# Performance work log

Hardware: AMD Instinct MI355X
Metric: run time of the kernel (lower is better)

## Reference

```python
import jax, jax.numpy as jnp
import numpy as np

NS = 0.4      # neighborhood_size
GS = 8        # grid_size
RNN = 128     # rnn_size
EMB = 64      # embedding_size
NMIX = 20     # nmixtures
N = 1024      # num pedestrians


def setup_inputs() -> dict:
    key = jax.random.key(0)
    ks = jax.random.split(key, 14)
    s = 0.05
    return {
        "xoff": jax.random.normal(ks[0], (N, 2)) * s,
        "xabs": jax.random.uniform(ks[1], (N, 2)),
        "h0": jax.random.normal(ks[2], (1, N, RNN)) * 0.1,
        "c0": jax.random.normal(ks[3], (1, N, RNN)) * 0.1,
        "W_emb": jax.random.normal(ks[4], (EMB, 2)) * s,
        "b_emb": jax.random.normal(ks[5], (EMB,)) * s,
        "W_soc": jax.random.normal(ks[6], (EMB, GS * GS * RNN)) * s,
        "b_soc": jax.random.normal(ks[7], (EMB,)) * s,
        "W_ih": jax.random.normal(ks[8], (4 * RNN, 2 * EMB)) * s,
        "W_hh": jax.random.normal(ks[9], (4 * RNN, RNN)) * s,
        "b_ih": jax.random.normal(ks[10], (4 * RNN,)) * s,
        "b_hh": jax.random.normal(ks[11], (4 * RNN,)) * s,
        "W_out": jax.random.normal(ks[12], (6 * NMIX, RNN)) * s,
        "b_out": jax.random.normal(ks[13], (6 * NMIX,)) * s,
    }


def grid_mask(xabs, dtype):
    # Vectorized getGridMask: [N, N, GS*GS] one-hot neighbor binning.
    x, y = xabs[:, 0], xabs[:, 1]
    dx = x[None, :] - (x[:, None] - NS / 2)  # other_x - width_low, [N, N]
    dy = y[None, :] - (y[:, None] - NS / 2)
    cx = jnp.floor(dx / NS * GS).astype(jnp.int32)
    cy = jnp.floor(dy / NS * GS).astype(jnp.int32)
    n = x.shape[0]
    valid = ((dx >= 0) & (dx < NS) & (dy >= 0) & (dy < NS)
             & (cx >= 0) & (cx < GS) & (cy >= 0) & (cy < GS)
             & ~jnp.eye(n, dtype=bool))
    cell = jnp.clip(cx + cy * GS, 0, GS * GS - 1)
    return jax.nn.one_hot(cell, GS * GS, dtype=dtype) * valid[..., None].astype(dtype)


def reference(xoff, xabs, h0, c0, W_emb, b_emb, W_soc, b_soc,
              W_ih, W_hh, b_ih, b_hh, W_out, b_out):
    n = xabs.shape[0]
    # predict_distance=True -> embed offsets
    emb = jax.nn.relu(xoff @ W_emb.T + b_emb)                 # [N, 64]
    grid = grid_mask(xabs, emb.dtype)                          # [N, N, 64]
    h = h0[0]                                                  # [N, 128]
    # getSocialTensor: scatter neighbor hidden states into grid bins
    social = jnp.einsum('nmg,mh->ngh', grid, h).reshape(n, GS * GS * RNN)
    pool = jax.nn.relu(social @ W_soc.T + b_soc)               # [N, 64]
    xin = jnp.concatenate([emb, pool], axis=-1)                # [N, 128]
    # single-step LSTM, torch gate order i, f, g, o
    gates = xin @ W_ih.T + h @ W_hh.T + b_ih + b_hh            # [N, 512]
    i, f, g, o = jnp.split(gates, 4, axis=-1)
    c = jax.nn.sigmoid(f) * c0[0] + jax.nn.sigmoid(i) * jnp.tanh(g)
    hn = jax.nn.sigmoid(o) * jnp.tanh(c)
    out = hn @ W_out.T + b_out                                 # [N, 120]
    mu1, mu2, ls1, ls2, rho, pi_logits = jnp.split(out, 6, axis=1)
    return (mu1, mu2, ls1, ls2, rho, pi_logits)
```

## Files before the change

### kernel.cpp

```cpp
#include <hip/hip_runtime.h>
#include <hip/hip_bf16.h>

#define NN_ 1024

#define U_WIHT   0
#define U_WHHT   65536
#define U_WOUT   131072
#define OFF_POOL 73728
#define U_HHI    278528
#define U_HLO    409600
#define U_SHI    540672
#define U_SLO    1064960
#define U_P      1589248

typedef __attribute__((ext_vector_type(8))) short short8;
typedef __attribute__((ext_vector_type(4))) float floatx4;

__device__ __forceinline__ float b2f_(unsigned short u) {
    return __uint_as_float(((unsigned)u) << 16);
}
__device__ __forceinline__ unsigned short f2bu(float f) {
    __hip_bfloat16 b = __float2bfloat16(f);
    return *(unsigned short*)&b;
}
__device__ __forceinline__ float ldin(const void* p, int i, int isbf) {
    return isbf ? b2f_(((const unsigned short*)p)[i]) : ((const float*)p)[i];
}
__device__ __forceinline__ int detect_bf16(const void* Wih, int tid) {
    unsigned wv = ((const unsigned*)Wih)[tid];
    unsigned e8 = (wv >> 7) & 0xFFu;
    return (__syncthreads_count((e8 >= 96u && e8 <= 134u) ? 1 : 0) > 128) ? 1 : 0;
}

__global__ void prep_kernel(const void* __restrict__ h0,
                            const void* __restrict__ Wsoc,
                            const void* __restrict__ Wih_det,
                            float* __restrict__ ws) {
    const int tid = threadIdx.x;
    const int isbf = detect_bf16(Wih_det, tid);
    unsigned short* u16 = (unsigned short*)ws;
    int t = blockIdx.x * 256 + tid;
    float x; int dhi, dlo;
    if (t < 131072) {
        x = ldin(h0, t, isbf);
        dhi = U_HHI + t; dlo = U_HLO + t;
    } else {
        int t2 = t - 131072;
        x = ldin(Wsoc, t2, isbf);
        dhi = U_SHI + t2; dlo = U_SLO + t2;
    }
    unsigned short hi = f2bu(x);
    u16[dhi] = hi;
    u16[dlo] = f2bu(x - b2f_(hi));
}

__global__ __launch_bounds__(256) void pgemm_kernel(float* __restrict__ ws,
                                                    int m0, int mcnt) {
    const unsigned short* u16 = (const unsigned short*)ws;
    const short* Hhi = (const short*)(u16 + U_HHI);
    const short* Hlo = (const short*)(u16 + U_HLO);
    const short* Shi = (const short*)(u16 + U_SHI);
    const short* Slo = (const short*)(u16 + U_SLO);
    unsigned short* P16 = (unsigned short*)ws + U_P;

    const int tid  = threadIdx.x;
    const int lane = tid & 63;
    const int wv   = tid >> 6;
    const int B    = blockIdx.y * 64 + blockIdx.x;
    const int mtiles = mcnt >> 4;
    const int mtile  = B % mtiles;
    const int cg     = B / mtiles;
    const int m = lane & 15;
    const int q = lane >> 4;
    const int abase = (m0 + mtile * 16 + m) * 128 + q * 8;
    short8 ah[4], al[4];
#pragma unroll
    for (int j = 0; j < 4; j++) {
        ah[j] = *(const short8*)(Hhi + abase + 32 * j);
        al[j] = *(const short8*)(Hlo + abase + 32 * j);
    }
    const int rowl = mtile * 16 + q * 4;
#pragma unroll
    for (int t = 0; t < 4; t++) {
        int n0 = cg * 256 + wv * 64 + t * 16;
        int nc = n0 + m;
        int e  = nc & 63, g = nc >> 6;
        int wb = e * 8192 + g * 128 + q * 8;
        short8 bh[4], bl[4];
#pragma unroll
        for (int j = 0; j < 4; j++) {
            bh[j] = *(const short8*)(Shi + wb + 32 * j);
            bl[j] = *(const short8*)(Slo + wb + 32 * j);
        }
        floatx4 c = {0.0f, 0.0f, 0.0f, 0.0f};
#pragma unroll
        for (int j = 0; j < 4; j++) c = __builtin_amdgcn_mfma_f32_16x16x32_bf16(ah[j], bh[j], c, 0, 0, 0);
#pragma unroll
        for (int j = 0; j < 4; j++) c = __builtin_amdgcn_mfma_f32_16x16x32_bf16(ah[j], bl[j], c, 0, 0, 0);
#pragma unroll
        for (int j = 0; j < 4; j++) c = __builtin_amdgcn_mfma_f32_16x16x32_bf16(al[j], bh[j], c, 0, 0, 0);
#pragma unroll
        for (int r = 0; r < 4; r++)
            P16[(rowl + r) * 4096 + n0 + m] = f2bu(c[r]);
    }
}

__global__ __launch_bounds__(256) void pool_kernel(const void* __restrict__ xabs,
                                                   const void* __restrict__ Wih,
                                                   const void* __restrict__ Whh,
                                                   const void* __restrict__ Wout,
                                                   float* __restrict__ ws,
                                                   int m0, int mcount, int first) {
    __shared__ int off[NN_];
    __shared__ int cnt_s;
    __shared__ float4 red4[16][16];
    const int tid = threadIdx.x;
    const int isbf = detect_bf16(Wih, tid);
    const int n = blockIdx.x;

    if (first && blockIdx.x < 144) {
        unsigned short* u16 = (unsigned short*)ws;
        int base = blockIdx.x * 1024;
        for (int i = tid; i < 1024; i += 256) {
            int t = base + i;
            float v;
            if (t < 65536)       { int k = t >> 9, j = t & 511;       v = ldin(Wih, j * 128 + k, isbf); }
            else if (t < 131072) { int t2 = t - 65536; int k = t2 >> 9, j = t2 & 511; v = ldin(Whh, j * 128 + k, isbf); }
            else                 { int t2 = t - 131072; int r = t2 >> 7, j = t2 & 127;
                                   v = (j < 120) ? ldin(Wout, j * 128 + r, isbf) : 0.0f; }
            u16[t] = f2bu(v);
        }
    }
    if (tid == 0) cnt_s = 0;
    __syncthreads();

    float xs = ldin(xabs, 2 * n, isbf)     - 0.2f;
    float ys = ldin(xabs, 2 * n + 1, isbf) - 0.2f;
    for (int i = tid; i < mcount; i += 256) {
        int m = m0 + i;
        float dx = ldin(xabs, 2 * m, isbf)     - xs;
        float dy = ldin(xabs, 2 * m + 1, isbf) - ys;
        int cx = (int)floorf(dx / 0.4f * 8.0f);
        int cy = (int)floorf(dy / 0.4f * 8.0f);
        bool valid = (dx >= 0.0f) && (dx < 0.4f) && (dy >= 0.0f) && (dy < 0.4f)
                  && (cx >= 0) && (cx < 8) && (cy >= 0) && (cy < 8) && (m != n);
        if (valid) {
            int idx = atomicAdd(&cnt_s, 1);
            off[idx] = i * 4096 + ((cy * 8 + cx) << 6);
        }
    }
    __syncthreads();
    const unsigned short* P16 = (const unsigned short*)ws + U_P;
    const int e4 = tid & 15, strm = tid >> 4;
    const int cc = cnt_s;
    float ax = 0.0f, ay = 0.0f, az = 0.0f, aw = 0.0f;
    for (int j = strm; j < cc; j += 16) {
        int o = off[j];
        ushort4 u = *(const ushort4*)(P16 + o + 4 * e4);
        ax += b2f_(u.x); ay += b2f_(u.y); az += b2f_(u.z); aw += b2f_(u.w);
    }
    red4[strm][e4] = make_float4(ax, ay, az, aw);
    __syncthreads();
    if (tid < 16) {
        float4 s = make_float4(0.0f, 0.0f, 0.0f, 0.0f);
#pragma unroll
        for (int s16 = 0; s16 < 16; s16++) {
            float4 r = red4[s16][tid];
            s.x += r.x; s.y += r.y; s.z += r.z; s.w += r.w;
        }
        float* pp = ws + OFF_POOL + n * 64 + 4 * tid;
        if (!first) { s.x += pp[0]; s.y += pp[1]; s.z += pp[2]; s.w += pp[3]; }
        *(float4*)pp = s;
    }
}

__global__ __launch_bounds__(256) void lstm_out_kernel(
        const void* __restrict__ xoff, const void* __restrict__ h0,
        const void* __restrict__ c0,   const void* __restrict__ W_emb,
        const void* __restrict__ b_emb, const void* __restrict__ b_soc,
        const void* __restrict__ b_ih, const void* __restrict__ b_hh,
        const void* __restrict__ b_out, const void* __restrict__ Wih_det,
        const float* __restrict__ ws, float* __restrict__ out) {
    __shared__ __align__(16) float xin[2][128];
    __shared__ __align__(16) float hs[2][128];
    __shared__ __align__(16) float gl[2][512];
    __shared__ __align__(16) float hnl[2][128];
    const int tid = threadIdx.x;
    const int isbf = detect_bf16(Wih_det, tid);
    const int n0 = blockIdx.x * 2;
    const unsigned short* u16 = (const unsigned short*)ws;
    if (tid < 128) {
        int nn = tid >> 6, e = tid & 63, n = n0 + nn;
        float v = fmaf(ldin(xoff, 2 * n, isbf),     ldin(W_emb, 2 * e, isbf),
                  fmaf(ldin(xoff, 2 * n + 1, isbf), ldin(W_emb, 2 * e + 1, isbf),
                       ldin(b_emb, e, isbf)));
        xin[nn][e] = fmaxf(v, 0.0f);
        xin[nn][64 + e] = fmaxf(ws[OFF_POOL + n * 64 + e] + ldin(b_soc, e, isbf), 0.0f);
    } else {
        int t = tid - 128;
    }
    {
        int nn = tid >> 7, k = tid & 127;
        hs[nn][k] = ldin(h0, (n0 + nn) * 128 + k, isbf);
    }
    __syncthreads();
    {
        const int j0 = 2 * tid, j1 = 2 * tid + 1;
        float ax[2] = {0, 0}, ay[2] = {0, 0};
        for (int k = 0; k < 128; k += 4) {
            union { float4 v; float f[4]; } xu[2], hu[2];
#pragma unroll
            for (int nn = 0; nn < 2; nn++) {
                xu[nn].v = *(const float4*)&xin[nn][k];
                hu[nn].v = *(const float4*)&hs[nn][k];
            }
#pragma unroll
            for (int kk = 0; kk < 4; kk++) {
                ushort2 wi = *(const ushort2*)(u16 + U_WIHT + (k + kk) * 512 + j0);
                ushort2 wh = *(const ushort2*)(u16 + U_WHHT + (k + kk) * 512 + j0);
                float wix = b2f_(wi.x), wiy = b2f_(wi.y);
                float whx = b2f_(wh.x), why = b2f_(wh.y);
#pragma unroll
                for (int nn = 0; nn < 2; nn++) {
                    float xk = xu[nn].f[kk], hk = hu[nn].f[kk];
                    ax[nn] = fmaf(xk, wix, ax[nn]); ax[nn] = fmaf(hk, whx, ax[nn]);
                    ay[nn] = fmaf(xk, wiy, ay[nn]); ay[nn] = fmaf(hk, why, ay[nn]);
                }
            }
        }
        float bb0 = ldin(b_ih, j0, isbf) + ldin(b_hh, j0, isbf);
        float bb1 = ldin(b_ih, j1, isbf) + ldin(b_hh, j1, isbf);
#pragma unroll
        for (int nn = 0; nn < 2; nn++) {
            gl[nn][j0] = ax[nn] + bb0;
            gl[nn][j1] = ay[nn] + bb1;
        }
    }
    __syncthreads();
    {
        int nn = tid >> 7, r = tid & 127;
        int n = n0 + nn;
        float iv = gl[nn][r], fv = gl[nn][r + 128], gv = gl[nn][r + 256], ov = gl[nn][r + 384];
        float si = 1.0f / (1.0f + expf(-iv));
        float sf = 1.0f / (1.0f + expf(-fv));
        float so = 1.0f / (1.0f + expf(-ov));
        float cc = sf * ldin(c0, n * 128 + r, isbf) + si * tanhf(gv);
        hnl[nn][r] = so * tanhf(cc);
    }
    __syncthreads();
    {
        int nn = tid >> 7, j = tid & 127;
        if (j < 120) {
            float acc = ldin(b_out, j, isbf);
            for (int r = 0; r < 128; r += 4) {
                float4 hq = *(const float4*)&hnl[nn][r];
                acc = fmaf(hq.x, b2f_(u16[U_WOUT + (r + 0) * 128 + j]), acc);
                acc = fmaf(hq.y, b2f_(u16[U_WOUT + (r + 1) * 128 + j]), acc);
                acc = fmaf(hq.z, b2f_(u16[U_WOUT + (r + 2) * 128 + j]), acc);
                acc = fmaf(hq.w, b2f_(u16[U_WOUT + (r + 3) * 128 + j]), acc);
            }
            int ch = j / 20, wc = j - ch * 20;
            out[ch * 20480 + (n0 + nn) * 20 + wc] = acc;
        }
    }
}

extern "C" void kernel_launch(void* const* d_in, const int* in_sizes, int n_in,
                              void* d_out, int out_size, void* d_ws, size_t ws_size,
                              hipStream_t stream) {
    const void* xoff  = d_in[0];
    const void* xabs  = d_in[1];
    const void* h0    = d_in[2];
    const void* c0    = d_in[3];
    const void* W_emb = d_in[4];
    const void* b_emb = d_in[5];
    const void* W_soc = d_in[6];
    const void* b_soc = d_in[7];
    const void* W_ih  = d_in[8];
    const void* W_hh  = d_in[9];
    const void* b_ih  = d_in[10];
    const void* b_hh  = d_in[11];
    const void* W_out = d_in[12];
    const void* b_out = d_in[13];
    float* ws = (float*)d_ws;
    float* out = (float*)d_out;

    long long availu = (long long)(ws_size / 2) - (long long)U_P;
    long long cll = availu / 4096;
    int C = (cll > 1024) ? 1024 : (int)cll;
    C &= ~63;
    if (C < 64) C = 64;

    prep_kernel<<<2560, 256, 0, stream>>>(h0, W_soc, W_ih, ws);
    for (int m0 = 0; m0 < NN_; m0 += C) {
        int cnt = (NN_ - m0 < C) ? (NN_ - m0) : C;
        pgemm_kernel<<<dim3(64, cnt / 64), 256, 0, stream>>>(ws, m0, cnt);
        pool_kernel<<<NN_, 256, 0, stream>>>(xabs, W_ih, W_hh, W_out, ws, m0, cnt,
                                             m0 == 0 ? 1 : 0);
    }
    lstm_out_kernel<<<512, 256, 0, stream>>>(xoff, h0, c0, W_emb, b_emb, b_soc,
                                             b_ih, b_hh, b_out, W_ih, ws, out);
}
```

Measured before the change: 133.9 us.

## Fuse bf16 split prep into GEMM and pooling into LSTM kernel

Result: no change. 132.7 us (-0.9%).

```diff
diff --git a/kernel.cpp b/kernel.cpp
--- a/kernel.cpp
+++ b/kernel.cpp
@@ -3,15 +3,10 @@
 
 #define NN_ 1024
 
-#define U_WIHT   0
-#define U_WHHT   65536
-#define U_WOUT   131072
-#define OFF_POOL 73728
-#define U_HHI    278528
-#define U_HLO    409600
-#define U_SHI    540672
-#define U_SLO    1064960
-#define U_P      1589248
+#define U_WIHT 0
+#define U_WHHT 65536
+#define U_WOUT 131072
+#define U_P    147456
 
 typedef __attribute__((ext_vector_type(8))) short short8;
 typedef __attribute__((ext_vector_type(4))) float floatx4;
@@ -31,66 +26,70 @@
     unsigned e8 = (wv >> 7) & 0xFFu;
     return (__syncthreads_count((e8 >= 96u && e8 <= 134u) ? 1 : 0) > 128) ? 1 : 0;
 }
-
-__global__ void prep_kernel(const void* __restrict__ h0,
-                            const void* __restrict__ Wsoc,
-                            const void* __restrict__ Wih_det,
-                            float* __restrict__ ws) {
+__device__ __forceinline__ void split8f(const float* p, short8& hi, short8& lo) {
+    const float4 f0 = *(const float4*)p;
+    const float4 f1 = *(const float4*)(p + 4);
+    float x[8] = {f0.x, f0.y, f0.z, f0.w, f1.x, f1.y, f1.z, f1.w};
+    unsigned short* H = (unsigned short*)&hi;
+    unsigned short* L = (unsigned short*)&lo;
+#pragma unroll
+    for (int i = 0; i < 8; i++) {
+        unsigned short h = f2bu(x[i]);
+        H[i] = h;
+        L[i] = f2bu(x[i] - b2f_(h));
+    }
+}
+
+__global__ __launch_bounds__(256) void pgemm_kernel(const void* __restrict__ Wsoc,
+                                                    const void* __restrict__ h0,
+                                                    const void* __restrict__ Wih,
+                                                    const void* __restrict__ Whh,
+                                                    const void* __restrict__ Wout,
+                                                    float* __restrict__ ws) {
     const int tid = threadIdx.x;
-    const int isbf = detect_bf16(Wih_det, tid);
-    unsigned short* u16 = (unsigned short*)ws;
-    int t = blockIdx.x * 256 + tid;
-    float x; int dhi, dlo;
-    if (t < 131072) {
-        x = ldin(h0, t, isbf);
-        dhi = U_HHI + t; dlo = U_HLO + t;
-    } else {
-        int t2 = t - 131072;
-        x = ldin(Wsoc, t2, isbf);
-        dhi = U_SHI + t2; dlo = U_SLO + t2;
-    }
-    unsigned short hi = f2bu(x);
-    u16[dhi] = hi;
-    u16[dlo] = f2bu(x - b2f_(hi));
-}
-
-__global__ __launch_bounds__(256) void pgemm_kernel(float* __restrict__ ws,
-                                                    int m0, int mcnt) {
-    const unsigned short* u16 = (const unsigned short*)ws;
-    const short* Hhi = (const short*)(u16 + U_HHI);
-    const short* Hlo = (const short*)(u16 + U_HLO);
-    const short* Shi = (const short*)(u16 + U_SHI);
-    const short* Slo = (const short*)(u16 + U_SLO);
-    unsigned short* P16 = (unsigned short*)ws + U_P;
-
-    const int tid  = threadIdx.x;
+    const int isbf = detect_bf16(Wih, tid);
+    unsigned short* u16w = (unsigned short*)ws;
+    unsigned short* P16  = u16w + U_P;
     const int lane = tid & 63;
     const int wv   = tid >> 6;
     const int B    = blockIdx.y * 64 + blockIdx.x;
-    const int mtiles = mcnt >> 4;
-    const int mtile  = B % mtiles;
-    const int cg     = B / mtiles;
+    const int mtile = B & 63;
+    const int cg    = B >> 6;
     const int m = lane & 15;
     const int q = lane >> 4;
-    const int abase = (m0 + mtile * 16 + m) * 128 + q * 8;
+    const int abase = (mtile * 16 + m) * 128 + q * 8;
     short8 ah[4], al[4];
-#pragma unroll
-    for (int j = 0; j < 4; j++) {
-        ah[j] = *(const short8*)(Hhi + abase + 32 * j);
-        al[j] = *(const short8*)(Hlo + abase + 32 * j);
+    if (isbf) {
+        const unsigned short* H = (const unsigned short*)h0;
+#pragma unroll
+        for (int j = 0; j < 4; j++) {
+            ah[j] = *(const short8*)(H + abase + 32 * j);
+            al[j] = short8{0, 0, 0, 0, 0, 0, 0, 0};
+        }
+    } else {
+        const float* H = (const float*)h0;
+#pragma unroll
+        for (int j = 0; j < 4; j++) split8f(H + abase + 32 * j, ah[j], al[j]);
     }
     const int rowl = mtile * 16 + q * 4;
 #pragma unroll
     for (int t = 0; t < 4; t++) {
-        int n0 = cg * 256 + wv * 64 + t * 16;
-        int nc = n0 + m;
-        int e  = nc & 63, g = nc >> 6;
-        int wb = e * 8192 + g * 128 + q * 8;
+        const int n0 = cg * 256 + wv * 64 + t * 16;
+        const int nc = n0 + m;
+        const int e = nc & 63, g = nc >> 6;
+        const int wb = e * 8192 + g * 128 + q * 8;
         short8 bh[4], bl[4];
-#pragma unroll
-        for (int j = 0; j < 4; j++) {
-            bh[j] = *(const short8*)(Shi + wb + 32 * j);
-            bl[j] = *(const short8*)(Slo + wb + 32 * j);
+        if (isbf) {
+            const unsigned short* W = (const unsigned short*)Wsoc;
+#pragma unroll
+            for (int j = 0; j < 4; j++) {
+                bh[j] = *(const short8*)(W + wb + 32 * j);
+                bl[j] = short8{0, 0, 0, 0, 0, 0, 0, 0};
+            }
+        } else {
+            const float* W = (const float*)Wsoc;
+#pragma unroll
+            for (int j = 0; j < 4; j++) split8f(W + wb + 32 * j, bh[j], bl[j]);
         }
         floatx4 c = {0.0f, 0.0f, 0.0f, 0.0f};
 #pragma unroll
@@ -103,24 +102,8 @@
         for (int r = 0; r < 4; r++)
             P16[(rowl + r) * 4096 + n0 + m] = f2bu(c[r]);
     }
-}
-
-__global__ __launch_bounds__(256) void pool_kernel(const void* __restrict__ xabs,
-                                                   const void* __restrict__ Wih,
-                                                   const void* __restrict__ Whh,
-                                                   const void* __restrict__ Wout,
-                                                   float* __restrict__ ws,
-                                                   int m0, int mcount, int first) {
-    __shared__ int off[NN_];
-    __shared__ int cnt_s;
-    __shared__ float4 red4[16][16];
-    const int tid = threadIdx.x;
-    const int isbf = detect_bf16(Wih, tid);
-    const int n = blockIdx.x;
-
-    if (first && blockIdx.x < 144) {
-        unsigned short* u16 = (unsigned short*)ws;
-        int base = blockIdx.x * 1024;
+    if (B < 144) {
+        int base = B * 1024;
         for (int i = tid; i < 1024; i += 256) {
             int t = base + i;
             float v;
@@ -128,59 +111,23 @@
             else if (t < 131072) { int t2 = t - 65536; int k = t2 >> 9, j = t2 & 511; v = ldin(Whh, j * 128 + k, isbf); }
             else                 { int t2 = t - 131072; int r = t2 >> 7, j = t2 & 127;
                                    v = (j < 120) ? ldin(Wout, j * 128 + r, isbf) : 0.0f; }
-            u16[t] = f2bu(v);
-        }
-    }
-    if (tid == 0) cnt_s = 0;
-    __syncthreads();
-
-    float xs = ldin(xabs, 2 * n, isbf)     - 0.2f;
-    float ys = ldin(xabs, 2 * n + 1, isbf) - 0.2f;
-    for (int i = tid; i < mcount; i += 256) {
-        int m = m0 + i;
-        float dx = ldin(xabs, 2 * m, isbf)     - xs;
-        float dy = ldin(xabs, 2 * m + 1, isbf) - ys;
-        int cx = (int)floorf(dx / 0.4f * 8.0f);
-        int cy = (int)floorf(dy / 0.4f * 8.0f);
-        bool valid = (dx >= 0.0f) && (dx < 0.4f) && (dy >= 0.0f) && (dy < 0.4f)
-                  && (cx >= 0) && (cx < 8) && (cy >= 0) && (cy < 8) && (m != n);
-        if (valid) {
-            int idx = atomicAdd(&cnt_s, 1);
-            off[idx] = i * 4096 + ((cy * 8 + cx) << 6);
-        }
-    }
-    __syncthreads();
-    const unsigned short* P16 = (const unsigned short*)ws + U_P;
-    const int e4 = tid & 15, strm = tid >> 4;
-    const int cc = cnt_s;
-    float ax = 0.0f, ay = 0.0f, az = 0.0f, aw = 0.0f;
-    for (int j = strm; j < cc; j += 16) {
-        int o = off[j];
-        ushort4 u = *(const ushort4*)(P16 + o + 4 * e4);
-        ax += b2f_(u.x); ay += b2f_(u.y); az += b2f_(u.z); aw += b2f_(u.w);
-    }
-    red4[strm][e4] = make_float4(ax, ay, az, aw);
-    __syncthreads();
-    if (tid < 16) {
-        float4 s = make_float4(0.0f, 0.0f, 0.0f, 0.0f);
-#pragma unroll
-        for (int s16 = 0; s16 < 16; s16++) {
-            float4 r = red4[s16][tid];
-            s.x += r.x; s.y += r.y; s.z += r.z; s.w += r.w;
-        }
-        float* pp = ws + OFF_POOL + n * 64 + 4 * tid;
-        if (!first) { s.x += pp[0]; s.y += pp[1]; s.z += pp[2]; s.w += pp[3]; }
-        *(float4*)pp = s;
-    }
-}
-
-__global__ __launch_bounds__(256) void lstm_out_kernel(
-        const void* __restrict__ xoff, const void* __restrict__ h0,
-        const void* __restrict__ c0,   const void* __restrict__ W_emb,
-        const void* __restrict__ b_emb, const void* __restrict__ b_soc,
-        const void* __restrict__ b_ih, const void* __restrict__ b_hh,
-        const void* __restrict__ b_out, const void* __restrict__ Wih_det,
+            u16w[t] = f2bu(v);
+        }
+    }
+}
+
+__global__ __launch_bounds__(256) void pool_lstm_kernel(
+        const void* __restrict__ xoff, const void* __restrict__ xabs,
+        const void* __restrict__ h0,   const void* __restrict__ c0,
+        const void* __restrict__ W_emb, const void* __restrict__ b_emb,
+        const void* __restrict__ b_soc, const void* __restrict__ b_ih,
+        const void* __restrict__ b_hh,  const void* __restrict__ b_out,
+        const void* __restrict__ Wih_det,
         const float* __restrict__ ws, float* __restrict__ out) {
+    __shared__ float xabs_s[2048];
+    __shared__ int   off[2][NN_];
+    __shared__ int   cnt_s[2];
+    __shared__ float4 red4[2][8][16];
     __shared__ __align__(16) float xin[2][128];
     __shared__ __align__(16) float hs[2][128];
     __shared__ __align__(16) float gl[2][512];
@@ -189,20 +136,65 @@
     const int isbf = detect_bf16(Wih_det, tid);
     const int n0 = blockIdx.x * 2;
     const unsigned short* u16 = (const unsigned short*)ws;
-    if (tid < 128) {
-        int nn = tid >> 6, e = tid & 63, n = n0 + nn;
+
+    for (int i = tid; i < 2048; i += 256) xabs_s[i] = ldin(xabs, i, isbf);
+    if (tid < 2) cnt_s[tid] = 0;
+    __syncthreads();
+
+    const int half = tid >> 7;
+    const int t2 = tid & 127;
+    const int n = n0 + half;
+    {
+        float xs = xabs_s[2 * n]     - 0.2f;
+        float ys = xabs_s[2 * n + 1] - 0.2f;
+        for (int i = t2; i < NN_; i += 128) {
+            float dx = xabs_s[2 * i]     - xs;
+            float dy = xabs_s[2 * i + 1] - ys;
+            int cx = (int)floorf(dx / 0.4f * 8.0f);
+            int cy = (int)floorf(dy / 0.4f * 8.0f);
+            bool valid = (dx >= 0.0f) && (dx < 0.4f) && (dy >= 0.0f) && (dy < 0.4f)
+                      && (cx >= 0) && (cx < 8) && (cy >= 0) && (cy < 8) && (i != n);
+            if (valid) {
+                int idx = atomicAdd(&cnt_s[half], 1);
+                off[half][idx] = i * 4096 + ((cy * 8 + cx) << 6);
+            }
+        }
+    }
+    __syncthreads();
+    {
+        const unsigned short* P16 = (const unsigned short*)ws + U_P;
+        const int strm = t2 >> 4, e4 = t2 & 15;
+        const int cc = cnt_s[half];
+        float ax = 0.0f, ay = 0.0f, az = 0.0f, aw = 0.0f;
+        for (int j = strm; j < cc; j += 8) {
+            int o = off[half][j];
+            ushort4 u = *(const ushort4*)(P16 + o + 4 * e4);
+            ax += b2f_(u.x); ay += b2f_(u.y); az += b2f_(u.z); aw += b2f_(u.w);
+        }
+        red4[half][strm][e4] = make_float4(ax, ay, az, aw);
+    }
+    __syncthreads();
+    if (t2 < 16) {
+        float4 s = make_float4(0.0f, 0.0f, 0.0f, 0.0f);
+#pragma unroll
+        for (int s8 = 0; s8 < 8; s8++) {
+            float4 r = red4[half][s8][t2];
+            s.x += r.x; s.y += r.y; s.z += r.z; s.w += r.w;
+        }
+        int e = 4 * t2;
+        xin[half][64 + e]     = fmaxf(s.x + ldin(b_soc, e,     isbf), 0.0f);
+        xin[half][64 + e + 1] = fmaxf(s.y + ldin(b_soc, e + 1, isbf), 0.0f);
+        xin[half][64 + e + 2] = fmaxf(s.z + ldin(b_soc, e + 2, isbf), 0.0f);
+        xin[half][64 + e + 3] = fmaxf(s.w + ldin(b_soc, e + 3, isbf), 0.0f);
+    }
+    if (t2 < 64) {
+        int e = t2;
         float v = fmaf(ldin(xoff, 2 * n, isbf),     ldin(W_emb, 2 * e, isbf),
                   fmaf(ldin(xoff, 2 * n + 1, isbf), ldin(W_emb, 2 * e + 1, isbf),
                        ldin(b_emb, e, isbf)));
-        xin[nn][e] = fmaxf(v, 0.0f);
-        xin[nn][64 + e] = fmaxf(ws[OFF_POOL + n * 64 + e] + ldin(b_soc, e, isbf), 0.0f);
-    } else {
-        int t = tid - 128;
-    }
-    {
-        int nn = tid >> 7, k = tid & 127;
-        hs[nn][k] = ldin(h0, (n0 + nn) * 128 + k, isbf);
-    }
+        xin[half][e] = fmaxf(v, 0.0f);
+    }
+    hs[half][t2] = ldin(h0, n * 128 + t2, isbf);
     __syncthreads();
     {
         const int j0 = 2 * tid, j1 = 2 * tid + 1;
@@ -238,29 +230,29 @@
     }
     __syncthreads();
     {
-        int nn = tid >> 7, r = tid & 127;
-        int n = n0 + nn;
-        float iv = gl[nn][r], fv = gl[nn][r + 128], gv = gl[nn][r + 256], ov = gl[nn][r + 384];
+        int r = t2;
+        float iv = gl[half][r], fv = gl[half][r + 128];
+        float gv = gl[half][r + 256], ov = gl[half][r + 384];
         float si = 1.0f / (1.0f + expf(-iv));
         float sf = 1.0f / (1.0f + expf(-fv));
         float so = 1.0f / (1.0f + expf(-ov));
         float cc = sf * ldin(c0, n * 128 + r, isbf) + si * tanhf(gv);
-        hnl[nn][r] = so * tanhf(cc);
-    }
-    __syncthreads();
-    {
-        int nn = tid >> 7, j = tid & 127;
+        hnl[half][r] = so * tanhf(cc);
+    }
+    __syncthreads();
+    {
+        int j = t2;
         if (j < 120) {
             float acc = ldin(b_out, j, isbf);
             for (int r = 0; r < 128; r += 4) {
-                float4 hq = *(const float4*)&hnl[nn][r];
+                float4 hq = *(const float4*)&hnl[half][r];
                 acc = fmaf(hq.x, b2f_(u16[U_WOUT + (r + 0) * 128 + j]), acc);
                 acc = fmaf(hq.y, b2f_(u16[U_WOUT + (r + 1) * 128 + j]), acc);
                 acc = fmaf(hq.z, b2f_(u16[U_WOUT + (r + 2) * 128 + j]), acc);
                 acc = fmaf(hq.w, b2f_(u16[U_WOUT + (r + 3) * 128 + j]), acc);
             }
             int ch = j / 20, wc = j - ch * 20;
-            out[ch * 20480 + (n0 + nn) * 20 + wc] = acc;
+            out[ch * 20480 + n * 20 + wc] = acc;
         }
     }
 }
@@ -285,19 +277,7 @@
     float* ws = (float*)d_ws;
     float* out = (float*)d_out;
 
-    long long availu = (long long)(ws_size / 2) - (long long)U_P;
-    long long cll = availu / 4096;
-    int C = (cll > 1024) ? 1024 : (int)cll;
-    C &= ~63;
-    if (C < 64) C = 64;
-
-    prep_kernel<<<2560, 256, 0, stream>>>(h0, W_soc, W_ih, ws);
-    for (int m0 = 0; m0 < NN_; m0 += C) {
-        int cnt = (NN_ - m0 < C) ? (NN_ - m0) : C;
-        pgemm_kernel<<<dim3(64, cnt / 64), 256, 0, stream>>>(ws, m0, cnt);
-        pool_kernel<<<NN_, 256, 0, stream>>>(xabs, W_ih, W_hh, W_out, ws, m0, cnt,
-                                             m0 == 0 ? 1 : 0);
-    }
-    lstm_out_kernel<<<512, 256, 0, stream>>>(xoff, h0, c0, W_emb, b_emb, b_soc,
-                                             b_ih, b_hh, b_out, W_ih, ws, out);
-}
+    pgemm_kernel<<<dim3(64, 16), 256, 0, stream>>>(W_soc, h0, W_ih, W_hh, W_out, ws);
+    pool_lstm_kernel<<<512, 256, 0, stream>>>(xoff, xabs, h0, c0, W_emb, b_emb,
+                                              b_soc, b_ih, b_hh, b_out, W_ih, ws, out);
+}
```
